# Kernel tuning notes

Hardware: AMD Instinct MI355X
Metric: run time of the kernel (lower is better)

The kernel has to match this reference:

```python
import jax, jax.numpy as jnp
import numpy as np

CHEBYSHEV_K = 5  # number of Chebyshev polynomial terms


def setup_inputs() -> dict:
    key = jax.random.key(0)
    k1, k2, k3 = jax.random.split(key, 3)
    B, N, F_in, F_out = 1024, 512, 16, 8
    x = jax.random.normal(k1, (B, N, F_in), dtype=jnp.float32)
    # symmetric scaled-Laplacian-like matrix, scaled small so recurrence stays stable
    A = jax.random.normal(k2, (N, N), dtype=jnp.float32) / jnp.sqrt(jnp.float32(N))
    L = 0.5 * (A + A.T)
    # xavier-uniform-like weights [K, F_in, F_out]
    limit = np.sqrt(6.0 / (F_in + F_out)).astype(np.float32)
    W = jax.random.uniform(k3, (CHEBYSHEV_K, F_in, F_out), dtype=jnp.float32,
                           minval=-limit, maxval=limit)
    b = jnp.zeros((F_out,), dtype=jnp.float32)
    return {"x": x, "L": L, "W": W, "b": b}


def reference(x, L, W, b):
    # x: [B, N, F_in], L: [N, N], W: [K, F_in, F_out], b: [F_out]
    Lx = lambda z: jnp.einsum('nm,bmf->bnf', L, z)
    Z0 = x
    Z1 = Lx(x)
    out = Z0 @ W[0] + Z1 @ W[1]
    for k in range(2, CHEBYSHEV_K):  # small fixed K, structural loop
        Zk = 2.0 * Lx(Z1) - Z0
        out = out + Zk @ W[k]
        Z0, Z1 = Z1, Zk
    return out + b
```

## Files before the change

kernel.cpp:

```cpp
#include <hip/hip_runtime.h>
#include <cstdint>
#include <cstddef>


typedef __attribute__((ext_vector_type(8))) short  frag_ab;
typedef __attribute__((ext_vector_type(4))) float  frag_cd;

constexpr int BN    = 512;
constexpr int FIN   = 16;
constexpr int FOUT  = 8;
constexpr int BT    = 4;
constexpr int NCOLS = BT * FIN;
constexpr int LDST  = BN + 8;
constexpr int ZBUF  = NCOLS * LDST;

__device__ __forceinline__ uint16_t f2bf(float f) {
    uint32_t u = __builtin_bit_cast(uint32_t, f);
    u += 0x7FFFu + ((u >> 16) & 1u);
    return (uint16_t)(u >> 16);
}
__device__ __forceinline__ float bf2f(uint16_t h) {
    uint32_t u = ((uint32_t)h) << 16;
    return __builtin_bit_cast(float, u);
}

__device__ __forceinline__ size_t aswz(int row, int k) {
    return ((size_t)((row >> 4) * 16 + (k >> 5)) * 64
            + ((k >> 3) & 3) * 16 + (row & 15)) * 8 + (k & 7);
}

__global__ void cvtL_rm(const float* __restrict__ Lf, uint16_t* __restrict__ Lb) {
    int i = blockIdx.x * 256 + threadIdx.x;
    Lb[i] = f2bf(Lf[i]);
}

__global__ __launch_bounds__(256)
void cvtL_swz(const float* __restrict__ Lf, uint16_t* __restrict__ Lb) {
    int t = blockIdx.x * 256 + threadIdx.x;
    int f = t >> 6, lane = t & 63;
    int mt = f >> 4, ks = f & 15;
    int row = mt * 16 + (lane & 15);
    int k0  = ks * 32 + (lane >> 4) * 8;
    const float4* p = reinterpret_cast<const float4*>(Lf + (size_t)row * BN + k0);
    float4 u0 = p[0], u1 = p[1];
    frag_ab o;
    o[0] = (short)f2bf(u0.x); o[1] = (short)f2bf(u0.y);
    o[2] = (short)f2bf(u0.z); o[3] = (short)f2bf(u0.w);
    o[4] = (short)f2bf(u1.x); o[5] = (short)f2bf(u1.y);
    o[6] = (short)f2bf(u1.z); o[7] = (short)f2bf(u1.w);
    *reinterpret_cast<frag_ab*>(Lb + (size_t)t * 8) = o;
}

__global__ __launch_bounds__(256)
void m2comp(const float* __restrict__ Lf, uint16_t* __restrict__ Mb) {
    const int tid = threadIdx.x;
    const int wv = tid >> 6, lane = tid & 63, lr = lane & 15, q = lane >> 4;
    const int i0 = (blockIdx.x >> 4) * 32 + (wv >> 1) * 16;
    const int j0 = (blockIdx.x & 15) * 32 + (wv & 1) * 16;
    frag_cd acc = {0.f, 0.f, 0.f, 0.f};
    const float* arow = Lf + (size_t)(i0 + lr) * BN;
    const float* brow = Lf + (size_t)(j0 + lr) * BN;
    for (int ks = 0; ks < 16; ++ks) {
        const int kb = ks * 32 + q * 8;
        const float4* ap = reinterpret_cast<const float4*>(arow + kb);
        const float4* bp = reinterpret_cast<const float4*>(brow + kb);
        float4 a0 = ap[0], a1 = ap[1], b0 = bp[0], b1 = bp[1];
        float av[8]  = {a0.x, a0.y, a0.z, a0.w, a1.x, a1.y, a1.z, a1.w};
        float bvv[8] = {b0.x, b0.y, b0.z, b0.w, b1.x, b1.y, b1.z, b1.w};
        frag_ab ah, al, bh, bl;
#pragma unroll
        for (int j = 0; j < 8; ++j) {
            uint16_t h = f2bf(av[j]);
            ah[j] = (short)h;
            al[j] = (short)f2bf(av[j] - bf2f(h));
            uint16_t g = f2bf(bvv[j]);
            bh[j] = (short)g;
            bl[j] = (short)f2bf(bvv[j] - bf2f(g));
        }
        acc = __builtin_amdgcn_mfma_f32_16x16x32_bf16(ah, bh, acc, 0, 0, 0);
        acc = __builtin_amdgcn_mfma_f32_16x16x32_bf16(ah, bl, acc, 0, 0, 0);
        acc = __builtin_amdgcn_mfma_f32_16x16x32_bf16(al, bh, acc, 0, 0, 0);
    }
#pragma unroll
    for (int r = 0; r < 4; ++r) {
        int i = i0 + q * 4 + r, j = j0 + lr;
        float v = 2.f * acc[r] - ((i == j) ? 1.f : 0.f);
        Mb[aswz(i, j)] = f2bf(v);
    }
}

__global__ __launch_bounds__(512, 2)
void cheb2_kernel(const float* __restrict__ x, const uint16_t* __restrict__ Lb,
                  const uint16_t* __restrict__ Mb, const float* __restrict__ W,
                  const float* __restrict__ bvec, float* __restrict__ out) {
    __shared__ uint16_t lds[2 * ZBUF];
    uint16_t* z0 = lds;
    uint16_t* z1 = lds + ZBUF;

    const int tid  = threadIdx.x;
    const int wave = tid >> 6;
    const int lane = tid & 63;
    const int lr   = lane & 15;
    const int q    = lane >> 4;

    const float4* x4 = reinterpret_cast<const float4*>(x + (size_t)blockIdx.x * (BT * BN * FIN));
    for (int s = 0; s < 2; ++s) {
        int a   = tid + s * 512;
        int f0g = a & 3;
        int n8  = (a >> 2) & 63;
        int bl  = a >> 8;
        int jb  = bl * 2048 + n8 * 32 + f0g;
        float4 v[8];
#pragma unroll
        for (int r = 0; r < 8; ++r) v[r] = x4[jb + r * 4];
        int cb = bl * 16 + f0g * 4;
        int nb = n8 * 8;
#pragma unroll
        for (int w = 0; w < 4; ++w) {
            frag_ab pk;
#pragma unroll
            for (int r = 0; r < 8; ++r)
                pk[r] = (short)f2bf(reinterpret_cast<const float*>(&v[r])[w]);
            *reinterpret_cast<frag_ab*>(&z0[(cb + w) * LDST + nb]) = pk;
        }
    }

    frag_ab wf[3];
#pragma unroll
    for (int p = 0; p < 3; ++p) {
        frag_ab t;
#pragma unroll
        for (int jj = 0; jj < 8; ++jj) {
            int k   = q * 8 + jj;
            int ki  = p * 2 + (k >> 4);
            int fin = k & 15;
            float val = 0.0f;
            if (lr < 8) {
                int idx = fin * FOUT + lr;
                if      (ki == 0) val = W[idx] - W[4 * (FIN * FOUT) + idx];
                else if (ki == 1) val = W[1 * (FIN * FOUT) + idx] - W[3 * (FIN * FOUT) + idx];
                else if (ki < 5)  val = W[ki * (FIN * FOUT) + idx];
            }
            t[jj] = (short)f2bf(val);
        }
        wf[p] = t;
    }
    const float bv = (lr < 8) ? bvec[lr] : 0.0f;

    frag_cd accOut[4][4] = {};

    auto loadA = [&](const uint16_t* M, int mt, int ks) -> frag_ab {
        return *reinterpret_cast<const frag_ab*>(
            M + ((size_t)(mt * 16 + ks) * 64 + lane) * 8);
    };

    frag_cd acc1[4][4];
    frag_cd acc2[4][4];

    auto round = [&](const uint16_t* cur) {
#pragma unroll
        for (int mi = 0; mi < 4; ++mi)
#pragma unroll
            for (int ct = 0; ct < 4; ++ct) {
                acc1[mi][ct] = (frag_cd){0.f, 0.f, 0.f, 0.f};
                acc2[mi][ct] = (frag_cd){0.f, 0.f, 0.f, 0.f};
            }
        for (int ks = 0; ks < 16; ++ks) {
            frag_ab bfr[4];
#pragma unroll
            for (int ct = 0; ct < 4; ++ct)
                bfr[ct] = *reinterpret_cast<const frag_ab*>(
                    cur + (ct * 16 + lr) * LDST + ks * 32 + q * 8);
#pragma unroll
            for (int mi = 0; mi < 4; ++mi) {
                frag_ab a = loadA(Lb, wave + mi * 8, ks);
                frag_ab m = loadA(Mb, wave + mi * 8, ks);
#pragma unroll
                for (int ct = 0; ct < 4; ++ct)
                    acc1[mi][ct] = __builtin_amdgcn_mfma_f32_16x16x32_bf16(
                        a, bfr[ct], acc1[mi][ct], 0, 0, 0);
#pragma unroll
                for (int ct = 0; ct < 4; ++ct)
                    acc2[mi][ct] = __builtin_amdgcn_mfma_f32_16x16x32_bf16(
                        m, bfr[ct], acc2[mi][ct], 0, 0, 0);
            }
        }
    };

    auto wb = [&](frag_cd (&acc)[4][4], uint16_t* dst, float scale) {
#pragma unroll
        for (int mi = 0; mi < 4; ++mi) {
            int row0 = (wave + mi * 8) * 16 + q * 4;
#pragma unroll
            for (int ct = 0; ct < 4; ++ct) {
                uint16_t* dp = dst + (ct * 16 + lr) * LDST + row0;
                ushort4 nv;
                nv.x = f2bf(scale * acc[mi][ct][0]);
                nv.y = f2bf(scale * acc[mi][ct][1]);
                nv.z = f2bf(scale * acc[mi][ct][2]);
                nv.w = f2bf(scale * acc[mi][ct][3]);
                *reinterpret_cast<ushort4*>(dp) = nv;
            }
        }
    };

    auto epi = [&](const uint16_t* bA, const uint16_t* bB, frag_ab wfr) {
        const uint16_t* base = (q < 2) ? bA : bB;
        int finb = (q & 1) * 8;
#pragma unroll
        for (int mi = 0; mi < 4; ++mi) {
            int n = (wave + mi * 8) * 16 + lr;
#pragma unroll
            for (int bt = 0; bt < 4; ++bt) {
                const uint16_t* pp = base + (bt * 16 + finb) * LDST + n;
                frag_ab afr;
#pragma unroll
                for (int jj = 0; jj < 8; ++jj) afr[jj] = (short)pp[jj * LDST];
                accOut[mi][bt] = __builtin_amdgcn_mfma_f32_16x16x32_bf16(
                    afr, wfr, accOut[mi][bt], 0, 0, 0);
            }
        }
    };

    __syncthreads();
    round(z0);
    wb(acc1, z1, 1.f);
    __syncthreads();
    epi(z0, z1, wf[0]);
    __syncthreads();
    wb(acc2, z0, 1.f);
    __syncthreads();
    round(z0);
    wb(acc1, z1, 2.f);
    __syncthreads();
    epi(z0, z1, wf[1]);
    __syncthreads();
    wb(acc2, z0, 2.f);
    __syncthreads();
    epi(z0, z0, wf[2]);

    float* fbuf = reinterpret_cast<float*>(z1);
    if (lr < 8) {
#pragma unroll
        for (int mi = 0; mi < 4; ++mi) {
            int n0 = (wave + mi * 8) * 16 + q * 4;
#pragma unroll
            for (int bt = 0; bt < 4; ++bt) {
#pragma unroll
                for (int r = 0; r < 4; ++r)
                    fbuf[(bt * BN + n0 + r) * FOUT + lr] = accOut[mi][bt][r] + bv;
            }
        }
    }
    __syncthreads();
    {
        const float4* fb4 = reinterpret_cast<const float4*>(fbuf);
        float4* o4 = reinterpret_cast<float4*>(out + (size_t)blockIdx.x * (BT * BN * FOUT));
#pragma unroll
        for (int i = 0; i < 8; ++i)
            o4[i * 512 + tid] = fb4[i * 512 + tid];
    }
}

template <bool LBF16>
__global__ __launch_bounds__(512, 2)
void cheb1_kernel(const float* __restrict__ x, const float* __restrict__ Lf,
                  const uint16_t* __restrict__ Lb, const float* __restrict__ W,
                  const float* __restrict__ bvec, float* __restrict__ out) {
    __shared__ uint16_t lds[2 * ZBUF];
    uint16_t* z0 = lds;
    uint16_t* z1 = lds + ZBUF;

    const int tid  = threadIdx.x;
    const int wave = tid >> 6;
    const int lane = tid & 63;
    const int lr   = lane & 15;
    const int q    = lane >> 4;

    const float4* x4 = reinterpret_cast<const float4*>(x + (size_t)blockIdx.x * (BT * BN * FIN));
    for (int s = 0; s < 2; ++s) {
        int a   = tid + s * 512;
        int f0g = a & 3;
        int n8  = (a >> 2) & 63;
        int bl  = a >> 8;
        int jb  = bl * 2048 + n8 * 32 + f0g;
        float4 v[8];
#pragma unroll
        for (int r = 0; r < 8; ++r) v[r] = x4[jb + r * 4];
        int cb = bl * 16 + f0g * 4;
        int nb = n8 * 8;
#pragma unroll
        for (int w = 0; w < 4; ++w) {
            frag_ab pk;
#pragma unroll
            for (int r = 0; r < 8; ++r)
                pk[r] = (short)f2bf(reinterpret_cast<const float*>(&v[r])[w]);
            *reinterpret_cast<frag_ab*>(&z0[(cb + w) * LDST + nb]) = pk;
        }
    }

    frag_ab wf[3];
#pragma unroll
    for (int p = 0; p < 3; ++p) {
        frag_ab t;
#pragma unroll
        for (int jj = 0; jj < 8; ++jj) {
            int k   = q * 8 + jj;
            int ki  = p * 2 + (k >> 4);
            int fin = k & 15;
            float val = (lr < 8 && ki < 5) ? W[ki * (FIN * FOUT) + fin * FOUT + lr] : 0.0f;
            t[jj] = (short)f2bf(val);
        }
        wf[p] = t;
    }
    const float bv = (lr < 8) ? bvec[lr] : 0.0f;

    frag_cd accOut[4][4] = {};

    auto loadA = [&](int mt, int ks) -> frag_ab {
        int row = mt * 16 + lr;
        int kb  = ks * 32 + q * 8;
        if constexpr (LBF16) {
            return *reinterpret_cast<const frag_ab*>(Lb + row * BN + kb);
        } else {
            const float4* p  = reinterpret_cast<const float4*>(Lf + row * BN + kb);
            float4 u0 = p[0], u1 = p[1];
            frag_ab t;
            t[0] = (short)f2bf(u0.x); t[1] = (short)f2bf(u0.y);
            t[2] = (short)f2bf(u0.z); t[3] = (short)f2bf(u0.w);
            t[4] = (short)f2bf(u1.x); t[5] = (short)f2bf(u1.y);
            t[6] = (short)f2bf(u1.z); t[7] = (short)f2bf(u1.w);
            return t;
        }
    };

    auto app = [&](const uint16_t* cur, uint16_t* dst, bool first) {
        frag_cd acc[4][4] = {};
        for (int ks = 0; ks < 16; ++ks) {
            frag_ab bfr[4];
#pragma unroll
            for (int ct = 0; ct < 4; ++ct)
                bfr[ct] = *reinterpret_cast<const frag_ab*>(
                    cur + (ct * 16 + lr) * LDST + ks * 32 + q * 8);
#pragma unroll
            for (int mi = 0; mi < 4; ++mi) {
                frag_ab a = loadA(wave + mi * 8, ks);
#pragma unroll
                for (int ct = 0; ct < 4; ++ct)
                    acc[mi][ct] = __builtin_amdgcn_mfma_f32_16x16x32_bf16(
                        a, bfr[ct], acc[mi][ct], 0, 0, 0);
            }
        }
#pragma unroll
        for (int mi = 0; mi < 4; ++mi) {
            int row0 = (wave + mi * 8) * 16 + q * 4;
#pragma unroll
            for (int ct = 0; ct < 4; ++ct) {
                uint16_t* dp = dst + (ct * 16 + lr) * LDST + row0;
                float pz[4] = {0.f, 0.f, 0.f, 0.f};
                if (!first) {
                    ushort4 pv = *reinterpret_cast<const ushort4*>(dp);
                    pz[0] = bf2f(pv.x); pz[1] = bf2f(pv.y);
                    pz[2] = bf2f(pv.z); pz[3] = bf2f(pv.w);
                }
                ushort4 nv;
                float v0 = acc[mi][ct][0], v1 = acc[mi][ct][1];
                float v2 = acc[mi][ct][2], v3 = acc[mi][ct][3];
                if (!first) {
                    v0 = 2.f * v0 - pz[0]; v1 = 2.f * v1 - pz[1];
                    v2 = 2.f * v2 - pz[2]; v3 = 2.f * v3 - pz[3];
                }
                nv.x = f2bf(v0); nv.y = f2bf(v1); nv.z = f2bf(v2); nv.w = f2bf(v3);
                *reinterpret_cast<ushort4*>(dp) = nv;
            }
        }
    };

    auto epi = [&](const uint16_t* bA, const uint16_t* bB, frag_ab wfr) {
        const uint16_t* base = (q < 2) ? bA : bB;
        int finb = (q & 1) * 8;
#pragma unroll
        for (int mi = 0; mi < 4; ++mi) {
            int n = (wave + mi * 8) * 16 + lr;
#pragma unroll
            for (int bt = 0; bt < 4; ++bt) {
                const uint16_t* pp = base + (bt * 16 + finb) * LDST + n;
                frag_ab afr;
#pragma unroll
                for (int jj = 0; jj < 8; ++jj) afr[jj] = (short)pp[jj * LDST];
                accOut[mi][bt] = __builtin_amdgcn_mfma_f32_16x16x32_bf16(
                    afr, wfr, accOut[mi][bt], 0, 0, 0);
            }
        }
    };

    __syncthreads();
    app(z0, z1, true);
    __syncthreads();
    epi(z0, z1, wf[0]);
    __syncthreads();
    app(z1, z0, false);
    __syncthreads();
    app(z0, z1, false);
    __syncthreads();
    epi(z0, z1, wf[1]);
    __syncthreads();
    app(z1, z0, false);
    __syncthreads();
    epi(z0, z0, wf[2]);

    if (lr < 8) {
        float* ob = out + (size_t)blockIdx.x * BT * BN * FOUT;
#pragma unroll
        for (int mi = 0; mi < 4; ++mi) {
            int row0 = (wave + mi * 8) * 16 + q * 4;
#pragma unroll
            for (int bt = 0; bt < 4; ++bt) {
                float* op = ob + bt * (BN * FOUT) + row0 * FOUT + lr;
                op[0 * FOUT] = accOut[mi][bt][0] + bv;
                op[1 * FOUT] = accOut[mi][bt][1] + bv;
                op[2 * FOUT] = accOut[mi][bt][2] + bv;
                op[3 * FOUT] = accOut[mi][bt][3] + bv;
            }
        }
    }
}

extern "C" void kernel_launch(void* const* d_in, const int* in_sizes, int n_in,
                              void* d_out, int out_size, void* d_ws, size_t ws_size,
                              hipStream_t stream) {
    const float* x  = (const float*)d_in[0];
    const float* Lf = (const float*)d_in[1];
    const float* W  = (const float*)d_in[2];
    const float* bv = (const float*)d_in[3];
    float* out = (float*)d_out;

    const size_t matB = (size_t)BN * BN * sizeof(uint16_t);

    if (ws_size >= 2 * matB) {
        uint16_t* Lb = (uint16_t*)d_ws;
        uint16_t* Mb = Lb + (size_t)BN * BN;
        cvtL_swz<<<dim3(128), dim3(256), 0, stream>>>(Lf, Lb);
        m2comp<<<dim3(256), dim3(256), 0, stream>>>(Lf, Mb);
        cheb2_kernel<<<dim3(256), dim3(512), 0, stream>>>(x, Lb, Mb, W, bv, out);
    } else if (ws_size >= matB) {
        uint16_t* Lb = (uint16_t*)d_ws;
        cvtL_rm<<<dim3(1024), dim3(256), 0, stream>>>(Lf, Lb);
        cheb1_kernel<true><<<dim3(256), dim3(512), 0, stream>>>(x, Lf, Lb, W, bv, out);
    } else {
        cheb1_kernel<false><<<dim3(256), dim3(512), 0, stream>>>(x, Lf, nullptr, W, bv, out);
    }
}
```

Measured before the change: 146.0 us.

## Halve per-block batch tile and split L/M passes to raise occupancy in cheb2

The cheb2 kernel now processes 2 batch items per block instead of 4 and launches 512 blocks. The fused round that accumulated L·Z and M·Z together is split into two sequential passes sharing one accumulator set. This cuts the accumulator register count and LDS footprint so launch bounds can request 4 blocks per SM, giving more parallel blocks and better latency hiding. In exchange, each L and M tile fetched from global/L2 is reused across fewer batch columns, so matrix traffic per unit of work roughly doubles.

Result: slower. 197.9 us (+35.6%).

```diff
diff --git a/kernel.cpp b/kernel.cpp
--- a/kernel.cpp
+++ b/kernel.cpp
@@ -9,10 +9,15 @@
 constexpr int BN    = 512;
 constexpr int FIN   = 16;
 constexpr int FOUT  = 8;
-constexpr int BT    = 4;
-constexpr int NCOLS = BT * FIN;
 constexpr int LDST  = BN + 8;
-constexpr int ZBUF  = NCOLS * LDST;
+
+constexpr int BT2   = 2;
+constexpr int NC2   = BT2 * FIN;
+constexpr int ZB2   = NC2 * LDST;
+
+constexpr int BT1   = 4;
+constexpr int NC1   = BT1 * FIN;
+constexpr int ZB1   = NC1 * LDST;
 
 __device__ __forceinline__ uint16_t f2bf(float f) {
     uint32_t u = __builtin_bit_cast(uint32_t, f);
@@ -89,13 +94,13 @@
     }
 }
 
-__global__ __launch_bounds__(512, 2)
+__global__ __launch_bounds__(512, 4)
 void cheb2_kernel(const float* __restrict__ x, const uint16_t* __restrict__ Lb,
                   const uint16_t* __restrict__ Mb, const float* __restrict__ W,
                   const float* __restrict__ bvec, float* __restrict__ out) {
-    __shared__ uint16_t lds[2 * ZBUF];
+    __shared__ uint16_t lds[2 * ZB2];
     uint16_t* z0 = lds;
-    uint16_t* z1 = lds + ZBUF;
+    uint16_t* z1 = lds + ZB2;
 
     const int tid  = threadIdx.x;
     const int wave = tid >> 6;
@@ -103,9 +108,9 @@
     const int lr   = lane & 15;
     const int q    = lane >> 4;
 
-    const float4* x4 = reinterpret_cast<const float4*>(x + (size_t)blockIdx.x * (BT * BN * FIN));
-    for (int s = 0; s < 2; ++s) {
-        int a   = tid + s * 512;
+    const float4* x4 = reinterpret_cast<const float4*>(x + (size_t)blockIdx.x * (BT2 * BN * FIN));
+    {
+        int a   = tid;
         int f0g = a & 3;
         int n8  = (a >> 2) & 63;
         int bl  = a >> 8;
@@ -147,52 +152,39 @@
     }
     const float bv = (lr < 8) ? bvec[lr] : 0.0f;
 
-    frag_cd accOut[4][4] = {};
-
-    auto loadA = [&](const uint16_t* M, int mt, int ks) -> frag_ab {
-        return *reinterpret_cast<const frag_ab*>(
-            M + ((size_t)(mt * 16 + ks) * 64 + lane) * 8);
-    };
-
-    frag_cd acc1[4][4];
-    frag_cd acc2[4][4];
-
-    auto round = [&](const uint16_t* cur) {
+    frag_cd accOut[4][BT2] = {};
+    frag_cd acc[4][BT2];
+
+    auto pass = [&](const uint16_t* Amat, const uint16_t* cur) {
 #pragma unroll
         for (int mi = 0; mi < 4; ++mi)
 #pragma unroll
-            for (int ct = 0; ct < 4; ++ct) {
-                acc1[mi][ct] = (frag_cd){0.f, 0.f, 0.f, 0.f};
-                acc2[mi][ct] = (frag_cd){0.f, 0.f, 0.f, 0.f};
-            }
+            for (int ct = 0; ct < BT2; ++ct)
+                acc[mi][ct] = (frag_cd){0.f, 0.f, 0.f, 0.f};
         for (int ks = 0; ks < 16; ++ks) {
-            frag_ab bfr[4];
-#pragma unroll
-            for (int ct = 0; ct < 4; ++ct)
+            frag_ab bfr[BT2];
+#pragma unroll
+            for (int ct = 0; ct < BT2; ++ct)
                 bfr[ct] = *reinterpret_cast<const frag_ab*>(
                     cur + (ct * 16 + lr) * LDST + ks * 32 + q * 8);
 #pragma unroll
             for (int mi = 0; mi < 4; ++mi) {
-                frag_ab a = loadA(Lb, wave + mi * 8, ks);
-                frag_ab m = loadA(Mb, wave + mi * 8, ks);
-#pragma unroll
-                for (int ct = 0; ct < 4; ++ct)
-                    acc1[mi][ct] = __builtin_amdgcn_mfma_f32_16x16x32_bf16(
-                        a, bfr[ct], acc1[mi][ct], 0, 0, 0);
-#pragma unroll
-                for (int ct = 0; ct < 4; ++ct)
-                    acc2[mi][ct] = __builtin_amdgcn_mfma_f32_16x16x32_bf16(
-                        m, bfr[ct], acc2[mi][ct], 0, 0, 0);
-            }
-        }
-    };
-
-    auto wb = [&](frag_cd (&acc)[4][4], uint16_t* dst, float scale) {
+                frag_ab a = *reinterpret_cast<const frag_ab*>(
+                    Amat + ((size_t)((wave + mi * 8) * 16 + ks) * 64 + lane) * 8);
+#pragma unroll
+                for (int ct = 0; ct < BT2; ++ct)
+                    acc[mi][ct] = __builtin_amdgcn_mfma_f32_16x16x32_bf16(
+                        a, bfr[ct], acc[mi][ct], 0, 0, 0);
+            }
+        }
+    };
+
+    auto wb = [&](uint16_t* dst, float scale) {
 #pragma unroll
         for (int mi = 0; mi < 4; ++mi) {
             int row0 = (wave + mi * 8) * 16 + q * 4;
 #pragma unroll
-            for (int ct = 0; ct < 4; ++ct) {
+            for (int ct = 0; ct < BT2; ++ct) {
                 uint16_t* dp = dst + (ct * 16 + lr) * LDST + row0;
                 ushort4 nv;
                 nv.x = f2bf(scale * acc[mi][ct][0]);
@@ -211,7 +203,7 @@
         for (int mi = 0; mi < 4; ++mi) {
             int n = (wave + mi * 8) * 16 + lr;
 #pragma unroll
-            for (int bt = 0; bt < 4; ++bt) {
+            for (int bt = 0; bt < BT2; ++bt) {
                 const uint16_t* pp = base + (bt * 16 + finb) * LDST + n;
                 frag_ab afr;
 #pragma unroll
@@ -223,19 +215,21 @@
     };
 
     __syncthreads();
-    round(z0);
-    wb(acc1, z1, 1.f);
+    pass(Lb, z0);
+    wb(z1, 1.f);
     __syncthreads();
     epi(z0, z1, wf[0]);
-    __syncthreads();
-    wb(acc2, z0, 1.f);
-    __syncthreads();
-    round(z0);
-    wb(acc1, z1, 2.f);
+    pass(Mb, z0);
+    __syncthreads();
+    wb(z0, 1.f);
+    __syncthreads();
+    pass(Lb, z0);
+    wb(z1, 2.f);
     __syncthreads();
     epi(z0, z1, wf[1]);
-    __syncthreads();
-    wb(acc2, z0, 2.f);
+    pass(Mb, z0);
+    __syncthreads();
+    wb(z0, 2.f);
     __syncthreads();
     epi(z0, z0, wf[2]);
 
@@ -245,7 +239,7 @@
         for (int mi = 0; mi < 4; ++mi) {
             int n0 = (wave + mi * 8) * 16 + q * 4;
 #pragma unroll
-            for (int bt = 0; bt < 4; ++bt) {
+            for (int bt = 0; bt < BT2; ++bt) {
 #pragma unroll
                 for (int r = 0; r < 4; ++r)
                     fbuf[(bt * BN + n0 + r) * FOUT + lr] = accOut[mi][bt][r] + bv;
@@ -255,9 +249,9 @@
     __syncthreads();
     {
         const float4* fb4 = reinterpret_cast<const float4*>(fbuf);
-        float4* o4 = reinterpret_cast<float4*>(out + (size_t)blockIdx.x * (BT * BN * FOUT));
-#pragma unroll
-        for (int i = 0; i < 8; ++i)
+        float4* o4 = reinterpret_cast<float4*>(out + (size_t)blockIdx.x * (BT2 * BN * FOUT));
+#pragma unroll
+        for (int i = 0; i < 4; ++i)
             o4[i * 512 + tid] = fb4[i * 512 + tid];
     }
 }
@@ -267,9 +261,9 @@
 void cheb1_kernel(const float* __restrict__ x, const float* __restrict__ Lf,
                   const uint16_t* __restrict__ Lb, const float* __restrict__ W,
                   const float* __restrict__ bvec, float* __restrict__ out) {
-    __shared__ uint16_t lds[2 * ZBUF];
+    __shared__ uint16_t lds[2 * ZB1];
     uint16_t* z0 = lds;
-    uint16_t* z1 = lds + ZBUF;
+    uint16_t* z1 = lds + ZB1;
 
     const int tid  = threadIdx.x;
     const int wave = tid >> 6;
@@ -277,7 +271,7 @@
     const int lr   = lane & 15;
     const int q    = lane >> 4;
 
-    const float4* x4 = reinterpret_cast<const float4*>(x + (size_t)blockIdx.x * (BT * BN * FIN));
+    const float4* x4 = reinterpret_cast<const float4*>(x + (size_t)blockIdx.x * (BT1 * BN * FIN));
     for (int s = 0; s < 2; ++s) {
         int a   = tid + s * 512;
         int f0g = a & 3;
@@ -410,7 +404,7 @@
     epi(z0, z0, wf[2]);
 
     if (lr < 8) {
-        float* ob = out + (size_t)blockIdx.x * BT * BN * FOUT;
+        float* ob = out + (size_t)blockIdx.x * BT1 * BN * FOUT;
 #pragma unroll
         for (int mi = 0; mi < 4; ++mi) {
             int row0 = (wave + mi * 8) * 16 + q * 4;
@@ -442,7 +436,7 @@
         uint16_t* Mb = Lb + (size_t)BN * BN;
         cvtL_swz<<<dim3(128), dim3(256), 0, stream>>>(Lf, Lb);
         m2comp<<<dim3(256), dim3(256), 0, stream>>>(Lf, Mb);
-        cheb2_kernel<<<dim3(256), dim3(512), 0, stream>>>(x, Lb, Mb, W, bv, out);
+        cheb2_kernel<<<dim3(512), dim3(512), 0, stream>>>(x, Lb, Mb, W, bv, out);
     } else if (ws_size >= matB) {
         uint16_t* Lb = (uint16_t*)d_ws;
         cvtL_rm<<<dim3(1024), dim3(256), 0, stream>>>(Lf, Lb);
```

## Precompute Chebyshev polynomial matrices and fold into single concatenated GEMM

Applied to the files above, without the earlier changes.

Builds T_k(L) matrices for k=0..4 in a fragment-swizzled concatenated buffer via small step kernels using hi/lo bf16 splits for L, projects x through each W_k first into a bf16 Y buffer, then computes the output as one GEMM over K=5*512 with double-buffered LDS tiles. This replaces the per-batch recurrence with a single large dense GEMM plus a projection pass. It trades the recurrence's repeated L applications for extra global traffic writing and reading Y, several extra launches, and reduced precision from rounding T_k to bf16.

Result: slower. 163.0 us (+11.6%).

```diff
diff --git a/kernel.cpp b/kernel.cpp
--- a/kernel.cpp
+++ b/kernel.cpp
@@ -6,13 +6,12 @@
 typedef __attribute__((ext_vector_type(8))) short  frag_ab;
 typedef __attribute__((ext_vector_type(4))) float  frag_cd;
 
-constexpr int BN    = 512;
-constexpr int FIN   = 16;
-constexpr int FOUT  = 8;
-constexpr int BT    = 4;
-constexpr int NCOLS = BT * FIN;
-constexpr int LDST  = BN + 8;
-constexpr int ZBUF  = NCOLS * LDST;
+constexpr int BN  = 512;
+constexpr int FIN = 16;
+constexpr int FOUT= 8;
+constexpr int GK  = 5 * BN;
+constexpr int LDST= BN + 8;
+constexpr int ZBUF= 64 * LDST;
 
 __device__ __forceinline__ uint16_t f2bf(float f) {
     uint32_t u = __builtin_bit_cast(uint32_t, f);
@@ -24,15 +23,229 @@
     return __builtin_bit_cast(float, u);
 }
 
+__device__ __forceinline__ size_t pfrag(int mt, int g, int lane) {
+    return ((size_t)(mt * 80 + g) * 64 + lane) * 8;
+}
+__device__ __forceinline__ size_t pelem(int k, int row, int col) {
+    return pfrag(row >> 4, k * 16 + (col >> 5),
+                 ((col >> 3) & 3) * 16 + (row & 15)) + (col & 7);
+}
+__device__ __forceinline__ size_t lfrag16(int mt, int kt, int lane) {
+    return ((size_t)(mt * 16 + kt) * 64 + lane) * 8;
+}
 __device__ __forceinline__ size_t aswz(int row, int k) {
-    return ((size_t)((row >> 4) * 16 + (k >> 5)) * 64
-            + ((k >> 3) & 3) * 16 + (row & 15)) * 8 + (k & 7);
-}
-
-__global__ void cvtL_rm(const float* __restrict__ Lf, uint16_t* __restrict__ Lb) {
-    int i = blockIdx.x * 256 + threadIdx.x;
-    Lb[i] = f2bf(Lf[i]);
-}
+    return lfrag16(row >> 4, k >> 5, ((k >> 3) & 3) * 16 + (row & 15)) + (k & 7);
+}
+
+
+__global__ __launch_bounds__(256)
+void cvtP(const float* __restrict__ Lf, uint16_t* __restrict__ Pcat,
+          uint16_t* __restrict__ Llo) {
+    int t = blockIdx.x * 256 + threadIdx.x;
+    int lane = t & 63, f = t >> 6;
+    int mt = f >> 4, kt = f & 15;
+    int row = mt * 16 + (lane & 15);
+    int k0  = kt * 32 + (lane >> 4) * 8;
+    const float4* p = reinterpret_cast<const float4*>(Lf + (size_t)row * BN + k0);
+    float4 u0 = p[0], u1 = p[1];
+    float v[8] = {u0.x, u0.y, u0.z, u0.w, u1.x, u1.y, u1.z, u1.w};
+    frag_ab hi, lo;
+#pragma unroll
+    for (int j = 0; j < 8; ++j) {
+        uint16_t h = f2bf(v[j]);
+        hi[j] = (short)h;
+        lo[j] = (short)f2bf(v[j] - bf2f(h));
+    }
+    *reinterpret_cast<frag_ab*>(Pcat + pfrag(mt, 16 + kt, lane)) = hi;
+    *reinterpret_cast<frag_ab*>(Llo + lfrag16(mt, kt, lane)) = lo;
+}
+
+__global__ __launch_bounds__(256)
+void pfill(uint16_t* __restrict__ Pcat) {
+    int t = blockIdx.x * 256 + threadIdx.x;
+    int lane = t & 63, f = t >> 6;
+    int mt = f >> 4, kt = f & 15;
+    int row = mt * 16 + (lane & 15);
+    int kb  = kt * 32 + (lane >> 4) * 8;
+    frag_ab o;
+#pragma unroll
+    for (int j = 0; j < 8; ++j) o[j] = (short)((row == kb + j) ? 0x3F80 : 0);
+    *reinterpret_cast<frag_ab*>(Pcat + pfrag(mt, kt, lane)) = o;
+}
+
+__global__ __launch_bounds__(256)
+void pstep(uint16_t* __restrict__ Pcat, const uint16_t* __restrict__ Llo,
+           int dstk, int srck, int subk) {
+    int tid = threadIdx.x, wv = tid >> 6, lane = tid & 63;
+    int lr = lane & 15, q = lane >> 4;
+    int it = blockIdx.x * 4 + wv;
+    int to = it >> 5, jt = it & 31;
+    frag_cd acc = {0.f, 0.f, 0.f, 0.f};
+    for (int ks = 0; ks < 16; ++ks) {
+        frag_ab ah = *reinterpret_cast<const frag_ab*>(Pcat + pfrag(to, 16 + ks, lane));
+        frag_ab al = *reinterpret_cast<const frag_ab*>(Llo + lfrag16(to, ks, lane));
+        frag_ab b  = *reinterpret_cast<const frag_ab*>(Pcat + pfrag(jt, srck * 16 + ks, lane));
+        acc = __builtin_amdgcn_mfma_f32_16x16x32_bf16(ah, b, acc, 0, 0, 0);
+        acc = __builtin_amdgcn_mfma_f32_16x16x32_bf16(al, b, acc, 0, 0, 0);
+    }
+#pragma unroll
+    for (int r = 0; r < 4; ++r) {
+        int row = to * 16 + q * 4 + r, col = jt * 16 + lr;
+        float s = (subk < 0) ? ((row == col) ? 1.f : 0.f)
+                             : bf2f(Pcat[pelem(subk, row, col)]);
+        Pcat[pelem(dstk, row, col)] = f2bf(2.f * acc[r] - s);
+    }
+}
+
+__global__ __launch_bounds__(256)
+void ycat(const float* __restrict__ x, const float* __restrict__ W,
+          uint16_t* __restrict__ Y) {
+    int tid = threadIdx.x;
+    int bb = tid >> 7, l = tid & 127;
+    int b = blockIdx.x * 2 + bb;
+    const float* xb = x + (size_t)b * (BN * FIN);
+    float xf[4][16];
+#pragma unroll
+    for (int mm = 0; mm < 4; ++mm)
+#pragma unroll
+        for (int fi = 0; fi < 4; ++fi) {
+            float4 u = *reinterpret_cast<const float4*>(xb + (size_t)(mm * 128 + l) * 16 + fi * 4);
+            xf[mm][fi * 4 + 0] = u.x; xf[mm][fi * 4 + 1] = u.y;
+            xf[mm][fi * 4 + 2] = u.z; xf[mm][fi * 4 + 3] = u.w;
+        }
+    uint16_t* yb = Y + (size_t)b * 8 * GK;
+#pragma unroll
+    for (int k = 0; k < 5; ++k) {
+#pragma unroll
+        for (int fo = 0; fo < 8; ++fo) {
+            float a0 = 0.f, a1 = 0.f, a2 = 0.f, a3 = 0.f;
+#pragma unroll
+            for (int f = 0; f < 16; ++f) {
+                float w = W[(k * 16 + f) * 8 + fo];
+                a0 += xf[0][f] * w; a1 += xf[1][f] * w;
+                a2 += xf[2][f] * w; a3 += xf[3][f] * w;
+            }
+            uint16_t* yr = yb + (size_t)fo * GK + k * 512 + l;
+            yr[0]   = f2bf(a0); yr[128] = f2bf(a1);
+            yr[256] = f2bf(a2); yr[384] = f2bf(a3);
+        }
+    }
+}
+
+__global__ __launch_bounds__(512, 2)
+void chebgemm(const uint16_t* __restrict__ Pcat, const uint16_t* __restrict__ Y,
+              const float* __restrict__ bvec, float* __restrict__ out) {
+    __shared__ uint16_t lds[34816];
+    uint16_t* a0 = lds;
+    uint16_t* a1 = lds + 8192;
+    uint16_t* b0 = lds + 16384;
+    uint16_t* b1 = lds + 25600;
+
+    int bid = blockIdx.x;
+    int wg  = (bid & 7) * 32 + (bid >> 3);
+    int mtB = wg >> 6;
+    int jtB = wg & 63;
+    int m0  = mtB * 128;
+    int j0  = jtB * 128;
+
+    int tid = threadIdx.x, wv = tid >> 6, lane = tid & 63;
+    int lr = lane & 15, q = lane >> 4;
+    int wm = wv >> 2, wj = wv & 3;
+
+    frag_cd acc[4][2] = {};
+    frag_ab rA[2], rB[2];
+
+    auto loadA = [&](int c) {
+#pragma unroll
+        for (int s = 0; s < 2; ++s) {
+            int idx = tid + s * 512;
+            int piece = idx >> 6, ln = idx & 63;
+            int amt = piece >> 1, kk = piece & 1;
+            rA[s] = *reinterpret_cast<const frag_ab*>(
+                Pcat + pfrag(mtB * 8 + amt, c * 2 + kk, ln));
+        }
+    };
+    auto loadB = [&](int c) {
+#pragma unroll
+        for (int s = 0; s < 2; ++s) {
+            int idx = tid + s * 512;
+            int jj = idx >> 3, c8 = idx & 7;
+            rB[s] = *reinterpret_cast<const frag_ab*>(
+                Y + (size_t)(j0 + jj) * GK + c * 64 + c8 * 8);
+        }
+    };
+    auto writeS = [&](uint16_t* ab, uint16_t* bb) {
+#pragma unroll
+        for (int s = 0; s < 2; ++s) {
+            int idx = tid + s * 512;
+            *reinterpret_cast<frag_ab*>(ab + (size_t)idx * 8) = rA[s];
+            int jj = idx >> 3, c8 = idx & 7;
+            *reinterpret_cast<frag_ab*>(bb + (size_t)jj * 72 + c8 * 8) = rB[s];
+        }
+    };
+    auto compute = [&](const uint16_t* ab, const uint16_t* bb) {
+#pragma unroll
+        for (int ksub = 0; ksub < 2; ++ksub) {
+            frag_ab aF[4], bF[2];
+#pragma unroll
+            for (int mi = 0; mi < 4; ++mi)
+                aF[mi] = *reinterpret_cast<const frag_ab*>(
+                    ab + (size_t)(((wm * 4 + mi) * 2 + ksub) * 64 + lane) * 8);
+#pragma unroll
+            for (int cj = 0; cj < 2; ++cj)
+                bF[cj] = *reinterpret_cast<const frag_ab*>(
+                    bb + (size_t)(wj * 32 + cj * 16 + lr) * 72 + ksub * 32 + q * 8);
+#pragma unroll
+            for (int mi = 0; mi < 4; ++mi)
+#pragma unroll
+                for (int cj = 0; cj < 2; ++cj)
+                    acc[mi][cj] = __builtin_amdgcn_mfma_f32_16x16x32_bf16(
+                        aF[mi], bF[cj], acc[mi][cj], 0, 0, 0);
+        }
+    };
+
+    loadA(0); loadB(0);
+    writeS(a0, b0);
+    __syncthreads();
+    for (int c = 0; c < 40; ++c) {
+        bool odd = (c & 1) != 0;
+        const uint16_t* ap = odd ? a1 : a0;
+        const uint16_t* bp = odd ? b1 : b0;
+        uint16_t* an = odd ? a0 : a1;
+        uint16_t* bn = odd ? b0 : b1;
+        if (c < 39) { loadA(c + 1); loadB(c + 1); }
+        compute(ap, bp);
+        if (c < 39) writeS(an, bn);
+        __syncthreads();
+    }
+
+    float* fbuf = reinterpret_cast<float*>(lds);
+#pragma unroll
+    for (int mi = 0; mi < 4; ++mi)
+#pragma unroll
+        for (int cj = 0; cj < 2; ++cj) {
+            int jl = wj * 32 + cj * 16 + lr;
+#pragma unroll
+            for (int r = 0; r < 4; ++r) {
+                int nl = wm * 64 + mi * 16 + q * 4 + r;
+                fbuf[nl * 128 + jl] = acc[mi][cj][r];
+            }
+        }
+    __syncthreads();
+    float4 bv0 = *reinterpret_cast<const float4*>(bvec);
+    float4 bv1 = *(reinterpret_cast<const float4*>(bvec) + 1);
+#pragma unroll
+    for (int i = 0; i < 8; ++i) {
+        int L = i * 2048 + tid * 4;
+        int bb = L >> 10, r = L & 1023, nn = r >> 3, fo = r & 7;
+        float4 v = *reinterpret_cast<const float4*>(fbuf + nn * 128 + bb * 8 + fo);
+        float4 bias = (fo & 4) ? bv1 : bv0;
+        v.x += bias.x; v.y += bias.y; v.z += bias.z; v.w += bias.w;
+        *reinterpret_cast<float4*>(out + (size_t)(j0 / 8 + bb) * 4096
+                                       + (size_t)(m0 + nn) * 8 + fo) = v;
+    }
+}
+
 
 __global__ __launch_bounds__(256)
 void cvtL_swz(const float* __restrict__ Lf, uint16_t* __restrict__ Lb) {
@@ -64,18 +277,16 @@
         const int kb = ks * 32 + q * 8;
         const float4* ap = reinterpret_cast<const float4*>(arow + kb);
         const float4* bp = reinterpret_cast<const float4*>(brow + kb);
-        float4 a0 = ap[0], a1 = ap[1], b0 = bp[0], b1 = bp[1];
-        float av[8]  = {a0.x, a0.y, a0.z, a0.w, a1.x, a1.y, a1.z, a1.w};
-        float bvv[8] = {b0.x, b0.y, b0.z, b0.w, b1.x, b1.y, b1.z, b1.w};
+        float4 A0 = ap[0], A1 = ap[1], B0 = bp[0], B1 = bp[1];
+        float av[8]  = {A0.x, A0.y, A0.z, A0.w, A1.x, A1.y, A1.z, A1.w};
+        float bw[8]  = {B0.x, B0.y, B0.z, B0.w, B1.x, B1.y, B1.z, B1.w};
         frag_ab ah, al, bh, bl;
 #pragma unroll
         for (int j = 0; j < 8; ++j) {
             uint16_t h = f2bf(av[j]);
-            ah[j] = (short)h;
-            al[j] = (short)f2bf(av[j] - bf2f(h));
-            uint16_t g = f2bf(bvv[j]);
-            bh[j] = (short)g;
-            bl[j] = (short)f2bf(bvv[j] - bf2f(g));
+            ah[j] = (short)h; al[j] = (short)f2bf(av[j] - bf2f(h));
+            uint16_t g = f2bf(bw[j]);
+            bh[j] = (short)g; bl[j] = (short)f2bf(bw[j] - bf2f(g));
         }
         acc = __builtin_amdgcn_mfma_f32_16x16x32_bf16(ah, bh, acc, 0, 0, 0);
         acc = __builtin_amdgcn_mfma_f32_16x16x32_bf16(ah, bl, acc, 0, 0, 0);
@@ -93,28 +304,21 @@
 void cheb2_kernel(const float* __restrict__ x, const uint16_t* __restrict__ Lb,
                   const uint16_t* __restrict__ Mb, const float* __restrict__ W,
                   const float* __restrict__ bvec, float* __restrict__ out) {
-    __shared__ uint16_t lds[2 * ZBUF];
-    uint16_t* z0 = lds;
-    uint16_t* z1 = lds + ZBUF;
-
-    const int tid  = threadIdx.x;
-    const int wave = tid >> 6;
-    const int lane = tid & 63;
-    const int lr   = lane & 15;
-    const int q    = lane >> 4;
-
-    const float4* x4 = reinterpret_cast<const float4*>(x + (size_t)blockIdx.x * (BT * BN * FIN));
+    __shared__ uint16_t ldsb[2 * ZBUF];
+    uint16_t* z0 = ldsb;
+    uint16_t* z1 = ldsb + ZBUF;
+    const int tid = threadIdx.x, wave = tid >> 6, lane = tid & 63;
+    const int lr = lane & 15, q = lane >> 4;
+
+    const float4* x4 = reinterpret_cast<const float4*>(x + (size_t)blockIdx.x * (4 * BN * FIN));
     for (int s = 0; s < 2; ++s) {
-        int a   = tid + s * 512;
-        int f0g = a & 3;
-        int n8  = (a >> 2) & 63;
-        int bl  = a >> 8;
-        int jb  = bl * 2048 + n8 * 32 + f0g;
+        int a = tid + s * 512;
+        int f0g = a & 3, n8 = (a >> 2) & 63, bl = a >> 8;
+        int jb = bl * 2048 + n8 * 32 + f0g;
         float4 v[8];
 #pragma unroll
         for (int r = 0; r < 8; ++r) v[r] = x4[jb + r * 4];
-        int cb = bl * 16 + f0g * 4;
-        int nb = n8 * 8;
+        int cb = bl * 16 + f0g * 4, nb = n8 * 8;
 #pragma unroll
         for (int w = 0; w < 4; ++w) {
             frag_ab pk;
@@ -124,38 +328,27 @@
             *reinterpret_cast<frag_ab*>(&z0[(cb + w) * LDST + nb]) = pk;
         }
     }
-
     frag_ab wf[3];
 #pragma unroll
     for (int p = 0; p < 3; ++p) {
         frag_ab t;
 #pragma unroll
         for (int jj = 0; jj < 8; ++jj) {
-            int k   = q * 8 + jj;
-            int ki  = p * 2 + (k >> 4);
-            int fin = k & 15;
+            int k = q * 8 + jj, ki = p * 2 + (k >> 4), fin = k & 15;
             float val = 0.0f;
             if (lr < 8) {
                 int idx = fin * FOUT + lr;
-                if      (ki == 0) val = W[idx] - W[4 * (FIN * FOUT) + idx];
-                else if (ki == 1) val = W[1 * (FIN * FOUT) + idx] - W[3 * (FIN * FOUT) + idx];
-                else if (ki < 5)  val = W[ki * (FIN * FOUT) + idx];
+                if      (ki == 0) val = W[idx] - W[4 * 128 + idx];
+                else if (ki == 1) val = W[128 + idx] - W[3 * 128 + idx];
+                else if (ki < 5)  val = W[ki * 128 + idx];
             }
             t[jj] = (short)f2bf(val);
         }
         wf[p] = t;
     }
     const float bv = (lr < 8) ? bvec[lr] : 0.0f;
-
     frag_cd accOut[4][4] = {};
-
-    auto loadA = [&](const uint16_t* M, int mt, int ks) -> frag_ab {
-        return *reinterpret_cast<const frag_ab*>(
-            M + ((size_t)(mt * 16 + ks) * 64 + lane) * 8);
-    };
-
-    frag_cd acc1[4][4];
-    frag_cd acc2[4][4];
+    frag_cd acc1[4][4], acc2[4][4];
 
     auto round = [&](const uint16_t* cur) {
 #pragma unroll
@@ -173,8 +366,10 @@
                     cur + (ct * 16 + lr) * LDST + ks * 32 + q * 8);
 #pragma unroll
             for (int mi = 0; mi < 4; ++mi) {
-                frag_ab a = loadA(Lb, wave + mi * 8, ks);
-                frag_ab m = loadA(Mb, wave + mi * 8, ks);
+                frag_ab a = *reinterpret_cast<const frag_ab*>(
+                    Lb + lfrag16(wave + mi * 8, ks, lane));
+                frag_ab m = *reinterpret_cast<const frag_ab*>(
+                    Mb + lfrag16(wave + mi * 8, ks, lane));
 #pragma unroll
                 for (int ct = 0; ct < 4; ++ct)
                     acc1[mi][ct] = __builtin_amdgcn_mfma_f32_16x16x32_bf16(
@@ -186,7 +381,6 @@
             }
         }
     };
-
     auto wb = [&](frag_cd (&acc)[4][4], uint16_t* dst, float scale) {
 #pragma unroll
         for (int mi = 0; mi < 4; ++mi) {
@@ -195,15 +389,12 @@
             for (int ct = 0; ct < 4; ++ct) {
                 uint16_t* dp = dst + (ct * 16 + lr) * LDST + row0;
                 ushort4 nv;
-                nv.x = f2bf(scale * acc[mi][ct][0]);
-                nv.y = f2bf(scale * acc[mi][ct][1]);
-                nv.z = f2bf(scale * acc[mi][ct][2]);
-                nv.w = f2bf(scale * acc[mi][ct][3]);
+                nv.x = f2bf(scale * acc[mi][ct][0]); nv.y = f2bf(scale * acc[mi][ct][1]);
+                nv.z = f2bf(scale * acc[mi][ct][2]); nv.w = f2bf(scale * acc[mi][ct][3]);
                 *reinterpret_cast<ushort4*>(dp) = nv;
             }
         }
     };
-
     auto epi = [&](const uint16_t* bA, const uint16_t* bB, frag_ab wfr) {
         const uint16_t* base = (q < 2) ? bA : bB;
         int finb = (q & 1) * 8;
@@ -245,50 +436,40 @@
         for (int mi = 0; mi < 4; ++mi) {
             int n0 = (wave + mi * 8) * 16 + q * 4;
 #pragma unroll
-            for (int bt = 0; bt < 4; ++bt) {
+            for (int bt = 0; bt < 4; ++bt)
 #pragma unroll
                 for (int r = 0; r < 4; ++r)
                     fbuf[(bt * BN + n0 + r) * FOUT + lr] = accOut[mi][bt][r] + bv;
-            }
         }
     }
     __syncthreads();
     {
         const float4* fb4 = reinterpret_cast<const float4*>(fbuf);
-        float4* o4 = reinterpret_cast<float4*>(out + (size_t)blockIdx.x * (BT * BN * FOUT));
+        float4* o4 = reinterpret_cast<float4*>(out + (size_t)blockIdx.x * (4 * BN * FOUT));
 #pragma unroll
         for (int i = 0; i < 8; ++i)
             o4[i * 512 + tid] = fb4[i * 512 + tid];
     }
 }
 
-template <bool LBF16>
 __global__ __launch_bounds__(512, 2)
 void cheb1_kernel(const float* __restrict__ x, const float* __restrict__ Lf,
-                  const uint16_t* __restrict__ Lb, const float* __restrict__ W,
-                  const float* __restrict__ bvec, float* __restrict__ out) {
-    __shared__ uint16_t lds[2 * ZBUF];
-    uint16_t* z0 = lds;
-    uint16_t* z1 = lds + ZBUF;
-
-    const int tid  = threadIdx.x;
-    const int wave = tid >> 6;
-    const int lane = tid & 63;
-    const int lr   = lane & 15;
-    const int q    = lane >> 4;
-
-    const float4* x4 = reinterpret_cast<const float4*>(x + (size_t)blockIdx.x * (BT * BN * FIN));
+                  const float* __restrict__ W, const float* __restrict__ bvec,
+                  float* __restrict__ out) {
+    __shared__ uint16_t ldsb[2 * ZBUF];
+    uint16_t* z0 = ldsb;
+    uint16_t* z1 = ldsb + ZBUF;
+    const int tid = threadIdx.x, wave = tid >> 6, lane = tid & 63;
+    const int lr = lane & 15, q = lane >> 4;
+    const float4* x4 = reinterpret_cast<const float4*>(x + (size_t)blockIdx.x * (4 * BN * FIN));
     for (int s = 0; s < 2; ++s) {
-        int a   = tid + s * 512;
-        int f0g = a & 3;
-        int n8  = (a >> 2) & 63;
-        int bl  = a >> 8;
-        int jb  = bl * 2048 + n8 * 32 + f0g;
+        int a = tid + s * 512;
+        int f0g = a & 3, n8 = (a >> 2) & 63, bl = a >> 8;
+        int jb = bl * 2048 + n8 * 32 + f0g;
         float4 v[8];
 #pragma unroll
         for (int r = 0; r < 8; ++r) v[r] = x4[jb + r * 4];
-        int cb = bl * 16 + f0g * 4;
-        int nb = n8 * 8;
+        int cb = bl * 16 + f0g * 4, nb = n8 * 8;
 #pragma unroll
         for (int w = 0; w < 4; ++w) {
             frag_ab pk;
@@ -298,42 +479,30 @@
             *reinterpret_cast<frag_ab*>(&z0[(cb + w) * LDST + nb]) = pk;
         }
     }
-
     frag_ab wf[3];
 #pragma unroll
     for (int p = 0; p < 3; ++p) {
         frag_ab t;
 #pragma unroll
         for (int jj = 0; jj < 8; ++jj) {
-            int k   = q * 8 + jj;
-            int ki  = p * 2 + (k >> 4);
-            int fin = k & 15;
-            float val = (lr < 8 && ki < 5) ? W[ki * (FIN * FOUT) + fin * FOUT + lr] : 0.0f;
+            int k = q * 8 + jj, ki = p * 2 + (k >> 4), fin = k & 15;
+            float val = (lr < 8 && ki < 5) ? W[ki * 128 + fin * FOUT + lr] : 0.0f;
             t[jj] = (short)f2bf(val);
         }
         wf[p] = t;
     }
     const float bv = (lr < 8) ? bvec[lr] : 0.0f;
-
     frag_cd accOut[4][4] = {};
-
     auto loadA = [&](int mt, int ks) -> frag_ab {
-        int row = mt * 16 + lr;
-        int kb  = ks * 32 + q * 8;
-        if constexpr (LBF16) {
-            return *reinterpret_cast<const frag_ab*>(Lb + row * BN + kb);
-        } else {
-            const float4* p  = reinterpret_cast<const float4*>(Lf + row * BN + kb);
-            float4 u0 = p[0], u1 = p[1];
-            frag_ab t;
-            t[0] = (short)f2bf(u0.x); t[1] = (short)f2bf(u0.y);
-            t[2] = (short)f2bf(u0.z); t[3] = (short)f2bf(u0.w);
-            t[4] = (short)f2bf(u1.x); t[5] = (short)f2bf(u1.y);
-            t[6] = (short)f2bf(u1.z); t[7] = (short)f2bf(u1.w);
-            return t;
-        }
-    };
-
+        const float4* p = reinterpret_cast<const float4*>(Lf + (size_t)(mt * 16 + lr) * BN + ks * 32 + q * 8);
+        float4 u0 = p[0], u1 = p[1];
+        frag_ab t;
+        t[0] = (short)f2bf(u0.x); t[1] = (short)f2bf(u0.y);
+        t[2] = (short)f2bf(u0.z); t[3] = (short)f2bf(u0.w);
+        t[4] = (short)f2bf(u1.x); t[5] = (short)f2bf(u1.y);
+        t[6] = (short)f2bf(u1.z); t[7] = (short)f2bf(u1.w);
+        return t;
+    };
     auto app = [&](const uint16_t* cur, uint16_t* dst, bool first) {
         frag_cd acc[4][4] = {};
         for (int ks = 0; ks < 16; ++ks) {
@@ -366,16 +535,13 @@
                 ushort4 nv;
                 float v0 = acc[mi][ct][0], v1 = acc[mi][ct][1];
                 float v2 = acc[mi][ct][2], v3 = acc[mi][ct][3];
-                if (!first) {
-                    v0 = 2.f * v0 - pz[0]; v1 = 2.f * v1 - pz[1];
-                    v2 = 2.f * v2 - pz[2]; v3 = 2.f * v3 - pz[3];
-                }
+                if (!first) { v0 = 2.f*v0-pz[0]; v1 = 2.f*v1-pz[1];
+                              v2 = 2.f*v2-pz[2]; v3 = 2.f*v3-pz[3]; }
                 nv.x = f2bf(v0); nv.y = f2bf(v1); nv.z = f2bf(v2); nv.w = f2bf(v3);
                 *reinterpret_cast<ushort4*>(dp) = nv;
             }
         }
     };
-
     auto epi = [&](const uint16_t* bA, const uint16_t* bB, frag_ab wfr) {
         const uint16_t* base = (q < 2) ? bA : bB;
         int finb = (q & 1) * 8;
@@ -393,34 +559,24 @@
             }
         }
     };
-
-    __syncthreads();
-    app(z0, z1, true);
-    __syncthreads();
-    epi(z0, z1, wf[0]);
-    __syncthreads();
-    app(z1, z0, false);
-    __syncthreads();
-    app(z0, z1, false);
-    __syncthreads();
-    epi(z0, z1, wf[1]);
-    __syncthreads();
-    app(z1, z0, false);
-    __syncthreads();
+    __syncthreads();
+    app(z0, z1, true);  __syncthreads();
+    epi(z0, z1, wf[0]); __syncthreads();
+    app(z1, z0, false); __syncthreads();
+    app(z0, z1, false); __syncthreads();
+    epi(z0, z1, wf[1]); __syncthreads();
+    app(z1, z0, false); __syncthreads();
     epi(z0, z0, wf[2]);
-
     if (lr < 8) {
-        float* ob = out + (size_t)blockIdx.x * BT * BN * FOUT;
+        float* ob = out + (size_t)blockIdx.x * 4 * BN * FOUT;
 #pragma unroll
         for (int mi = 0; mi < 4; ++mi) {
             int row0 = (wave + mi * 8) * 16 + q * 4;
 #pragma unroll
             for (int bt = 0; bt < 4; ++bt) {
                 float* op = ob + bt * (BN * FOUT) + row0 * FOUT + lr;
-                op[0 * FOUT] = accOut[mi][bt][0] + bv;
-                op[1 * FOUT] = accOut[mi][bt][1] + bv;
-                op[2 * FOUT] = accOut[mi][bt][2] + bv;
-                op[3 * FOUT] = accOut[mi][bt][3] + bv;
+                op[0] = accOut[mi][bt][0] + bv; op[FOUT] = accOut[mi][bt][1] + bv;
+                op[2 * FOUT] = accOut[mi][bt][2] + bv; op[3 * FOUT] = accOut[mi][bt][3] + bv;
             }
         }
     }
@@ -435,19 +591,29 @@
     const float* bv = (const float*)d_in[3];
     float* out = (float*)d_out;
 
-    const size_t matB = (size_t)BN * BN * sizeof(uint16_t);
-
-    if (ws_size >= 2 * matB) {
+    const size_t PCAT_B = (size_t)32 * 80 * 64 * 8 * 2;
+    const size_t LLO_B  = (size_t)BN * BN * 2;
+    const size_t YC_B   = (size_t)8192 * GK * 2;
+    const size_t matB   = (size_t)BN * BN * 2;
+
+    if (ws_size >= PCAT_B + LLO_B + YC_B) {
+        uint16_t* Pcat = (uint16_t*)d_ws;
+        uint16_t* Llo  = Pcat + PCAT_B / 2;
+        uint16_t* Yc   = Pcat + (PCAT_B + LLO_B) / 2;
+        cvtP  <<<dim3(128), dim3(256), 0, stream>>>(Lf, Pcat, Llo);
+        pfill <<<dim3(128), dim3(256), 0, stream>>>(Pcat);
+        pstep <<<dim3(256), dim3(256), 0, stream>>>(Pcat, Llo, 2, 1, -1);
+        pstep <<<dim3(256), dim3(256), 0, stream>>>(Pcat, Llo, 3, 2, 1);
+        pstep <<<dim3(256), dim3(256), 0, stream>>>(Pcat, Llo, 4, 3, 2);
+        ycat  <<<dim3(512), dim3(256), 0, stream>>>(x, W, Yc);
+        chebgemm<<<dim3(256), dim3(512), 0, stream>>>(Pcat, Yc, bv, out);
+    } else if (ws_size >= 2 * matB) {
         uint16_t* Lb = (uint16_t*)d_ws;
         uint16_t* Mb = Lb + (size_t)BN * BN;
         cvtL_swz<<<dim3(128), dim3(256), 0, stream>>>(Lf, Lb);
-        m2comp<<<dim3(256), dim3(256), 0, stream>>>(Lf, Mb);
+        m2comp  <<<dim3(256), dim3(256), 0, stream>>>(Lf, Mb);
         cheb2_kernel<<<dim3(256), dim3(512), 0, stream>>>(x, Lb, Mb, W, bv, out);
-    } else if (ws_size >= matB) {
-        uint16_t* Lb = (uint16_t*)d_ws;
-        cvtL_rm<<<dim3(1024), dim3(256), 0, stream>>>(Lf, Lb);
-        cheb1_kernel<true><<<dim3(256), dim3(512), 0, stream>>>(x, Lf, Lb, W, bv, out);
     } else {
-        cheb1_kernel<false><<<dim3(256), dim3(512), 0, stream>>>(x, Lf, nullptr, W, bv, out);
-    }
-}
+        cheb1_kernel<<<dim3(256), dim3(512), 0, stream>>>(x, Lf, W, bv, out);
+    }
+}
```
